# Kernel tuning notes

Hardware: AMD Instinct MI355X
Metric: run time of the kernel (lower is better)

## Reference

```python
import jax, jax.numpy as jnp
import numpy as np

N_A = 50000   # 'user' nodes
N_B = 50000   # 'item' nodes
E = 1000000   # edges per relation
IN, HID, OUT = 128, 128, 64


def setup_inputs() -> dict:
    key = jax.random.key(0)
    ks = jax.random.split(key, 24)
    def glorot(k, shape):
        scale = 1.0 / np.sqrt(shape[0])
        return jax.random.normal(k, shape, jnp.float32) * scale
    inp = {
        "feat_A": jax.random.normal(ks[0], (N_A, IN), jnp.float32),
        "feat_B": jax.random.normal(ks[1], (N_B, IN), jnp.float32),
        "rates_src": jax.random.randint(ks[2], (E,), 0, N_A, jnp.int32),
        "rates_dst": jax.random.randint(ks[3], (E,), 0, N_B, jnp.int32),
        "ratedby_src": jax.random.randint(ks[4], (E,), 0, N_B, jnp.int32),
        "ratedby_dst": jax.random.randint(ks[5], (E,), 0, N_A, jnp.int32),
        "follows_src": jax.random.randint(ks[6], (E,), 0, N_A, jnp.int32),
        "follows_dst": jax.random.randint(ks[7], (E,), 0, N_A, jnp.int32),
        "neg_src": jax.random.randint(ks[8], (E,), 0, N_A, jnp.int32),
        "neg_dst": jax.random.randint(ks[9], (E,), 0, N_B, jnp.int32),
        "W1_rates": glorot(ks[10], (IN, HID)),   "b1_rates": jnp.zeros((HID,), jnp.float32),
        "W1_ratedby": glorot(ks[11], (IN, HID)), "b1_ratedby": jnp.zeros((HID,), jnp.float32),
        "W1_follows": glorot(ks[12], (IN, HID)), "b1_follows": jnp.zeros((HID,), jnp.float32),
        "W2_rates": glorot(ks[13], (HID, OUT)),   "b2_rates": jnp.zeros((OUT,), jnp.float32),
        "W2_ratedby": glorot(ks[14], (HID, OUT)), "b2_ratedby": jnp.zeros((OUT,), jnp.float32),
        "W2_follows": glorot(ks[15], (HID, OUT)), "b2_follows": jnp.zeros((OUT,), jnp.float32),
    }
    return inp


def _graph_conv(x_src, W, b, src, dst, n_src, n_dst):
    # DGL GraphConv, norm='both': D_dst^{-1/2} A D_src^{-1/2} (X W) + b
    ones = jnp.ones(src.shape[0], x_src.dtype)
    deg_out = jnp.maximum(jax.ops.segment_sum(ones, src, num_segments=n_src), 1.0)
    deg_in = jnp.maximum(jax.ops.segment_sum(ones, dst, num_segments=n_dst), 1.0)
    h = (x_src * (deg_out ** -0.5)[:, None]) @ W          # [n_src, d_out]
    agg = jax.ops.segment_sum(h[src], dst, num_segments=n_dst)  # SpMM
    return agg * (deg_in ** -0.5)[:, None] + b


def reference(feat_A, feat_B,
              W1_rates, b1_rates, W1_ratedby, b1_ratedby, W1_follows, b1_follows,
              W2_rates, b2_rates, W2_ratedby, b2_ratedby, W2_follows, b2_follows,
              rates_src, rates_dst, ratedby_src, ratedby_dst,
              follows_src, follows_dst, neg_src, neg_dst):
    # --- RGCN layer 1 (HeteroGraphConv, aggregate='sum') ---
    hB = _graph_conv(feat_A, W1_rates, b1_rates, rates_src, rates_dst, N_A, N_B)
    hA = (_graph_conv(feat_B, W1_ratedby, b1_ratedby, ratedby_src, ratedby_dst, N_B, N_A)
          + _graph_conv(feat_A, W1_follows, b1_follows, follows_src, follows_dst, N_A, N_A))
    hA = jax.nn.relu(hA)
    hB = jax.nn.relu(hB)
    # --- RGCN layer 2 ---
    oB = _graph_conv(hA, W2_rates, b2_rates, rates_src, rates_dst, N_A, N_B)
    oA = (_graph_conv(hB, W2_ratedby, b2_ratedby, ratedby_src, ratedby_dst, N_B, N_A)
          + _graph_conv(hA, W2_follows, b2_follows, follows_src, follows_dst, N_A, N_A))
    # --- HeteroInnerProduct (u_dot_v on etype 'rates') for pos and neg graphs ---
    pos_score = jnp.sum(oA[rates_src] * oB[rates_dst], axis=1, keepdims=True)  # [E, 1]
    neg_score = jnp.sum(oA[neg_src] * oB[neg_dst], axis=1, keepdims=True)      # [E, 1]
    return pos_score, neg_score
```

## Files before the change

kernel.cpp:

```cpp
#include <hip/hip_runtime.h>
#include <hip/hip_fp16.h>
#include <cstddef>
#include <type_traits>

#define N_NODES 50000
#define E_EDGES 1000000
#define NBUCK 196
#define ACHUNK 3907
#define MTILES 3125
#define HB 96
#define HCHUNK 10417
#define GB1 384
#define GB2 256

typedef _Float16 f16x8 __attribute__((ext_vector_type(8)));
typedef float f32x4 __attribute__((ext_vector_type(4)));

__global__ __launch_bounds__(256) void fused0(
        const float* __restrict__ w0, const float* __restrict__ w1,
        const float* __restrict__ w2, const float* __restrict__ w3,
        const float* __restrict__ w4, const float* __restrict__ w5,
        __half* __restrict__ Wt,
        const int* __restrict__ rs, const int* __restrict__ rd,
        const int* __restrict__ bs, const int* __restrict__ bd,
        const int* __restrict__ fs, const int* __restrict__ fd,
        int* __restrict__ bphist) {
    int bx = blockIdx.x;
    if (bx < 6 * HB) {
        __shared__ int l[NBUCK];
        int arr = bx / HB, blk = bx % HB;
        const int* idx = arr == 0 ? rs : arr == 1 ? rd : arr == 2 ? bs
                       : arr == 3 ? bd : arr == 4 ? fs : fd;
        for (int b = threadIdx.x; b < NBUCK; b += 256) l[b] = 0;
        __syncthreads();
        int e0 = blk * HCHUNK;
        int e1 = e0 + HCHUNK; if (e1 > E_EDGES) e1 = E_EDGES;
        for (int i = e0 + threadIdx.x; i < e1; i += 256)
            atomicAdd(&l[((unsigned)idx[i]) >> 8], 1);
        __syncthreads();
        int* dst = bphist + (size_t)(arr * HB + blk) * NBUCK;
        for (int b = threadIdx.x; b < NBUCK; b += 256) dst[b] = l[b];
        return;
    }
    bx -= 6 * HB;
    int m = bx / 16, part = bx % 16;
    const float* W = m == 0 ? w0 : m == 1 ? w1 : m == 2 ? w2 : m == 3 ? w3 : m == 4 ? w4 : w5;
    __half* Tt = Wt + (m < 3 ? m * 16384 : 49152 + (m - 3) * 8192);
    int ncol = m < 3 ? 128 : 64;
    int tot = 128 * ncol;
    for (int i = part * 256 + threadIdx.x; i < tot; i += 16 * 256) {
        int n = i >> 7, k = i & 127;
        Tt[i] = __float2half(W[k * ncol + n]);
    }
}

__global__ void bucket_scan_par(const int* __restrict__ bphist, int* __restrict__ gbase,
                                int* __restrict__ gcur) {
    int arr = blockIdx.x;
    int t = threadIdx.x;
    int c = 0;
    if (t < NBUCK) {
        const int* p = bphist + (size_t)arr * HB * NBUCK + t;
#pragma unroll 8
        for (int blk = 0; blk < HB; blk++) c += p[(size_t)blk * NBUCK];
    }
    int lane = t & 63, wid = t >> 6;
    __shared__ int wsum[4];
    int v = c;
#pragma unroll
    for (int o = 1; o < 64; o <<= 1) { int u = __shfl_up(v, o); if (lane >= o) v += u; }
    if (lane == 63) wsum[wid] = v;
    __syncthreads();
    int base = 0;
    for (int ww = 0; ww < wid; ww++) base += wsum[ww];
    int excl = base + v - c;
    if (t < NBUCK) {
        gbase[arr * (NBUCK + 1) + t] = excl;
        gcur[arr * NBUCK + t] = excl;
    }
    if (t == 255) gbase[arr * (NBUCK + 1) + NBUCK] = base + v;
}

__global__ __launch_bounds__(256) void fused_bin(
        const int* __restrict__ rs, const int* __restrict__ rd,
        const int* __restrict__ bs, const int* __restrict__ bd,
// ... 20 lines not shown
        }
        __syncthreads();
        unsigned* pp = pairs + (size_t)rel * E_EDGES;
        for (int i = e0 + threadIdx.x; i < e1; i += 256) {
            int d = dst[i];
            int b = ((unsigned)d) >> 8;
            int p = lbase[b] + atomicAdd(&lcnt[b], 1);
            pp[p] = ((unsigned)(d & 255) << 16) | (unsigned)src[i];
        }
    } else {
        int rel = y - 3, arr = 2 * rel;
        const int* src = rel == 0 ? rs : rel == 1 ? bs : fs;
        for (int i = e0 + threadIdx.x; i < e1; i += 256)
            atomicAdd(&lcnt[((unsigned)src[i]) >> 8], 1);
        __syncthreads();
        for (int b = threadIdx.x; b < NBUCK; b += 256) {
            lbase[b] = lcnt[b] ? atomicAdd(&gcur[arr * NBUCK + b], lcnt[b]) : 0;
            lcnt[b] = 0;
        }
        __syncthreads();
        unsigned char* sb = sbytes + (size_t)rel * E_EDGES;
        for (int i = e0 + threadIdx.x; i < e1; i += 256) {
            int s = src[i];
            int b = ((unsigned)s) >> 8;
            int p = lbase[b] + atomicAdd(&lcnt[b], 1);
            sb[p] = (unsigned char)(s & 255);
        }
    }
}

__global__ __launch_bounds__(256) void fused_finish(
        const unsigned* __restrict__ pairs, const unsigned char* __restrict__ sbytes,
        const int* __restrict__ gbase, int* __restrict__ row_ptr,
        float* __restrict__ scales, int* __restrict__ col) {
    int y = blockIdx.y, b = blockIdx.x, t = threadIdx.x;
    __shared__ int cnt[256];
    __shared__ int rowbase[256];
    __shared__ int wsum[4];
    if (y < 3) {
        int rel = y, arr = 2 * rel;
        int p0 = gbase[arr * (NBUCK + 1) + b];
        int p1 = gbase[arr * (NBUCK + 1) + b + 1];
        const unsigned char* sb = sbytes + (size_t)rel * E_EDGES;
        cnt[t] = 0;
        __syncthreads();
        for (int i = p0 + t; i < p1; i += 256)
            atomicAdd(&cnt[sb[i]], 1);
        __syncthreads();
        int node = b * 256 + t;
        if (node < N_NODES) {
            int c = cnt[t]; if (c < 1) c = 1;
            scales[(size_t)arr * N_NODES + node] = 1.0f / sqrtf((float)c);
        }
    } else {
        int rel = y - 3, arr = 2 * rel + 1;
        int gb = gbase[arr * (NBUCK + 1) + b];
        int ge = gbase[arr * (NBUCK + 1) + b + 1];
        const unsigned* pp = pairs + (size_t)rel * E_EDGES;
        cnt[t] = 0;
        __syncthreads();
        for (int i = gb + t; i < ge; i += 256)
            atomicAdd(&cnt[pp[i] >> 16], 1);
        __syncthreads();
        int lane = t & 63, wid = t >> 6;
        int c0 = cnt[t];
        int v = c0;
#pragma unroll
        for (int o = 1; o < 64; o <<= 1) { int u = __shfl_up(v, o); if (lane >= o) v += u; }
        if (lane == 63) wsum[wid] = v;
        __syncthreads();
        int base = gb;
        for (int w = 0; w < wid; w++) base += wsum[w];
        int excl = base + v - c0;
        rowbase[t] = excl;
        int node = b * 256 + t;
        if (node <= N_NODES)
            row_ptr[(size_t)rel * (N_NODES + 1) + node] = excl;
        if (node < N_NODES) {
            int c = c0; if (c < 1) c = 1;
            scales[(size_t)arr * N_NODES + node] = 1.0f / sqrtf((float)c);
        }
        cnt[t] = 0;
        __syncthreads();
        int* cl = col + (size_t)rel * E_EDGES;
        for (int i = gb + t; i < ge; i += 256) {
            unsigned p = pp[i];
            int dl = p >> 16;
            int slot = rowbase[dl] + atomicAdd(&cnt[dl], 1);
            cl[slot] = (int)(p & 0xFFFFu);
        }
    }
}

template <int NCOL, typename XT>
__device__ __forceinline__ void gemm_body(const XT* __restrict__ X,
                                          const float* __restrict__ sc,
                                          const __half* __restrict__ Wt,
                                          __half* __restrict__ T,
                                          int bxr, int nblocks) {
    constexpr int NHALF = NCOL / 64;
    int gw = bxr * 4 + ((int)threadIdx.x >> 6);
    int lane = threadIdx.x & 63;
    int half_id = gw % NHALF;
    int mstream = gw / NHALF;
    int nstreams = nblocks * 4 / NHALF;
    int l15 = lane & 15, g = lane >> 4;

    f16x8 b[4][4];
    {
        const __half* wb = Wt + ((size_t)half_id * 64 + l15) * 128 + g * 8;
#pragma unroll
        for (int nt = 0; nt < 4; nt++)
#pragma unroll
            for (int kb = 0; kb < 4; kb++)
                b[nt][kb] = *(const f16x8*)(wb + nt * 16 * 128 + kb * 32);
    }

    for (int mt = mstream; mt < MTILES; mt += nstreams) {
        int m0 = mt * 16;
        f16x8 a[4];
        if constexpr (std::is_same<XT, float>::value) {
            const float* xr = X + (size_t)(m0 + l15) * 128 + g * 8;
#pragma unroll
            for (int kb = 0; kb < 4; kb++) {
                float4 u = *(const float4*)(xr + kb * 32);
                float4 v = *(const float4*)(xr + kb * 32 + 4);
                f16x8 t;
                t[0] = (_Float16)u.x; t[1] = (_Float16)u.y;
                t[2] = (_Float16)u.z; t[3] = (_Float16)u.w;
                t[4] = (_Float16)v.x; t[5] = (_Float16)v.y;
                t[6] = (_Float16)v.z; t[7] = (_Float16)v.w;
                a[kb] = t;
            }
        } else {
            const _Float16* xr = (const _Float16*)X + (size_t)(m0 + l15) * 128 + g * 8;
#pragma unroll
            for (int kb = 0; kb < 4; kb++)
                a[kb] = *(const f16x8*)(xr + kb * 32);
        }
        f32x4 acc[4];
#pragma unroll
        for (int nt = 0; nt < 4; nt++) acc[nt] = (f32x4){0.f, 0.f, 0.f, 0.f};
#pragma unroll
        for (int kb = 0; kb < 4; kb++)
#pragma unroll
            for (int nt = 0; nt < 4; nt++)
                acc[nt] = __builtin_amdgcn_mfma_f32_16x16x32_f16(a[kb], b[nt][kb], acc[nt], 0, 0, 0);
        int mrow = m0 + g * 4;
#pragma unroll
        for (int j = 0; j < 4; j++) {
            float sj = sc[mrow + j];
            __half* tj = T + (size_t)(mrow + j) * NCOL + half_id * 64 + l15;
            tj[0]  = __float2half(acc[0][j] * sj);
            tj[16] = __float2half(acc[1][j] * sj);
            tj[32] = __float2half(acc[2][j] * sj);
            tj[48] = __float2half(acc[3][j] * sj);
        }
    }
}

__global__ __launch_bounds__(256) void gemm_l1(const float* __restrict__ fA,
                                               const float* __restrict__ fB,
                                               const float* __restrict__ scales,
                                               const __half* __restrict__ Wt,
                                               __half* __restrict__ T012) {
    int rel = blockIdx.x / GB1, bxr = blockIdx.x % GB1;
    const float* X = (rel == 1) ? fB : fA;
    const float* sc = scales + (rel == 0 ? 0 : rel == 1 ? 2 * N_NODES : 4 * N_NODES);
    const __half* W = Wt + rel * 16384;
    __half* T = T012 + (size_t)rel * N_NODES * 128;
    gemm_body<128, float>(X, sc, W, T, bxr, GB1);
}

__global__ __launch_bounds__(256) void gemm_l2(const __half* __restrict__ hA,
                                               const __half* __restrict__ hB,
                                               const float* __restrict__ scales,
                                               const __half* __restrict__ Wt,
                                               __half* __restrict__ Tp) {
    int rel = blockIdx.x / GB2, bxr = blockIdx.x % GB2;
    const __half* X = (rel == 1) ? hB : hA;
    const float* sc = scales + (rel == 0 ? 0 : rel == 1 ? 2 * N_NODES : 4 * N_NODES);
    const __half* W = Wt + 49152 + rel * 8192;
    __half* T = Tp + (size_t)rel * N_NODES * 64;
    gemm_body<64, __half>(X, sc, W, T, bxr, GB2);
}

__global__ __launch_bounds__(256) void spmm_l1(
        const int* __restrict__ row_ptr, const int* __restrict__ col,
        const __half* __restrict__ T012, const float* __restrict__ scales,
        const float* __restrict__ b1r, const float* __restrict__ b1rb,
        const float* __restrict__ b1f,
        __half* __restrict__ hB, __half* __restrict__ hA) {
    int w = (blockIdx.x * blockDim.x + threadIdx.x) >> 6;
    int lane = threadIdx.x & 63;
    unsigned loff = (unsigned)lane << 2;
    const char* T0 = (const char*)T012;
    const char* T1 = T0 + (size_t)N_NODES * 256;
    const char* T2 = T1 + (size_t)N_NODES * 256;
#define LDT(B, c) __half22float2(*(const __half2*)((B) + (((unsigned)(c) << 8) + loff)))
    if (w < N_NODES / 2) {
        const int* cl = col;
        int rowA = w * 2, rowB = rowA + 1;
        int eA = row_ptr[rowA], EA = row_ptr[rowA + 1];
        int eB = EA, EB = row_ptr[rowB + 1];
        float axA = 0.f, ayA = 0.f, axB = 0.f, ayB = 0.f;
        while (eA + 4 <= EA && eB + 4 <= EB) {
            int a0 = cl[eA], a1 = cl[eA+1], a2 = cl[eA+2], a3 = cl[eA+3];
            int b0 = cl[eB], b1 = cl[eB+1], b2 = cl[eB+2], b3 = cl[eB+3];
            float2 v0 = LDT(T0, a0), v1 = LDT(T0, a1), v2 = LDT(T0, a2), v3 = LDT(T0, a3);
            float2 u0 = LDT(T0, b0), u1 = LDT(T0, b1), u2 = LDT(T0, b2), u3 = LDT(T0, b3);
            axA += (v0.x + v1.x) + (v2.x + v3.x); ayA += (v0.y + v1.y) + (v2.y + v3.y);
            axB += (u0.x + u1.x) + (u2.x + u3.x); ayB += (u0.y + u1.y) + (u2.y + u3.y);
            eA += 4; eB += 4;
        }
        while (eA + 4 <= EA) {
            int a0 = cl[eA], a1 = cl[eA+1], a2 = cl[eA+2], a3 = cl[eA+3];
            float2 v0 = LDT(T0, a0), v1 = LDT(T0, a1), v2 = LDT(T0, a2), v3 = LDT(T0, a3);
            axA += (v0.x + v1.x) + (v2.x + v3.x); ayA += (v0.y + v1.y) + (v2.y + v3.y);
            eA += 4;
        }
        while (eB + 4 <= EB) {
            int b0 = cl[eB], b1 = cl[eB+1], b2 = cl[eB+2], b3 = cl[eB+3];
            float2 u0 = LDT(T0, b0), u1 = LDT(T0, b1), u2 = LDT(T0, b2), u3 = LDT(T0, b3);
            axB += (u0.x + u1.x) + (u2.x + u3.x); ayB += (u0.y + u1.y) + (u2.y + u3.y);
            eB += 4;
        }
        while (eA < EA && eB < EB) {
            float2 v = LDT(T0, cl[eA]), u = LDT(T0, cl[eB]);
            axA += v.x; ayA += v.y; axB += u.x; ayB += u.y;
            eA++; eB++;
        }
        for (; eA < EA; eA++) { float2 v = LDT(T0, cl[eA]); axA += v.x; ayA += v.y; }
        for (; eB < EB; eB++) { float2 v = LDT(T0, cl[eB]); axB += v.x; ayB += v.y; }
        float bx = b1r[2 * lane], by = b1r[2 * lane + 1];
        float sA = scales[N_NODES + rowA], sB = scales[N_NODES + rowB];
        float ox = fmaxf(fmaf(axA, sA, bx), 0.f), oy = fmaxf(fmaf(ayA, sA, by), 0.f);
        *(__half2*)(hB + (size_t)rowA * 128 + 2 * lane) = __floats2half2_rn(ox, oy);
        ox = fmaxf(fmaf(axB, sB, bx), 0.f); oy = fmaxf(fmaf(ayB, sB, by), 0.f);
        *(__half2*)(hB + (size_t)rowB * 128 + 2 * lane) = __floats2half2_rn(ox, oy);
    } else {
        int r = w - N_NODES / 2;
        const int* rp1 = row_ptr + (N_NODES + 1);
        const int* rp2 = row_ptr + 2 * (N_NODES + 1);
        const int* cl1 = col + E_EDGES;
        const int* cl2 = col + 2 * (size_t)E_EDGES;
        int e1 = rp1[r], E1 = rp1[r + 1];
        int e2 = rp2[r], E2 = rp2[r + 1];
        float a1x = 0.f, a1y = 0.f, a2x = 0.f, a2y = 0.f;
        while (e1 + 4 <= E1 && e2 + 4 <= E2) {
            int a0 = cl1[e1], a1 = cl1[e1+1], a2 = cl1[e1+2], a3 = cl1[e1+3];
            int b0 = cl2[e2], b1 = cl2[e2+1], b2 = cl2[e2+2], b3 = cl2[e2+3];
            float2 v0 = LDT(T1, a0), v1 = LDT(T1, a1), v2 = LDT(T1, a2), v3 = LDT(T1, a3);
            float2 u0 = LDT(T2, b0), u1 = LDT(T2, b1), u2 = LDT(T2, b2), u3 = LDT(T2, b3);
            a1x += (v0.x + v1.x) + (v2.x + v3.x); a1y += (v0.y + v1.y) + (v2.y + v3.y);
            a2x += (u0.x + u1.x) + (u2.x + u3.x); a2y += (u0.y + u1.y) + (u2.y + u3.y);
            e1 += 4; e2 += 4;
        }
        while (e1 + 4 <= E1) {
            int a0 = cl1[e1], a1 = cl1[e1+1], a2 = cl1[e1+2], a3 = cl1[e1+3];
            float2 v0 = LDT(T1, a0), v1 = LDT(T1, a1), v2 = LDT(T1, a2), v3 = LDT(T1, a3);
            a1x += (v0.x + v1.x) + (v2.x + v3.x); a1y += (v0.y + v1.y) + (v2.y + v3.y);
            e1 += 4;
        }
        while (e2 + 4 <= E2) {
            int b0 = cl2[e2], b1 = cl2[e2+1], b2 = cl2[e2+2], b3 = cl2[e2+3];
            float2 u0 = LDT(T2, b0), u1 = LDT(T2, b1), u2 = LDT(T2, b2), u3 = LDT(T2, b3);
            a2x += (u0.x + u1.x) + (u2.x + u3.x); a2y += (u0.y + u1.y) + (u2.y + u3.y);
            e2 += 4;
        }
        while (e1 < E1 && e2 < E2) {
            float2 v = LDT(T1, cl1[e1]), u = LDT(T2, cl2[e2]);
            a1x += v.x; a1y += v.y; a2x += u.x; a2y += u.y;
            e1++; e2++;
        }
        for (; e1 < E1; e1++) { float2 v = LDT(T1, cl1[e1]); a1x += v.x; a1y += v.y; }
        for (; e2 < E2; e2++) { float2 v = LDT(T2, cl2[e2]); a2x += v.x; a2y += v.y; }
        float s1 = scales[3 * N_NODES + r], s2 = scales[5 * N_NODES + r];
        float ox = a1x * s1 + a2x * s2 + b1rb[2 * lane] + b1f[2 * lane];
        float oy = a1y * s1 + a2y * s2 + b1rb[2 * lane + 1] + b1f[2 * lane + 1];
        ox = fmaxf(ox, 0.f); oy = fmaxf(oy, 0.f);
        *(__half2*)(hA + (size_t)r * 128 + 2 * lane) = __floats2half2_rn(ox, oy);
    }
#undef LDT
}

__global__ __launch_bounds__(256) void spmm_l2(
        const int* __restrict__ row_ptr, const int* __restrict__ col,
        const __half* __restrict__ Tp, const float* __restrict__ scales,
        const float* __restrict__ b2r, const float* __restrict__ b2rb,
        const float* __restrict__ b2f,
        __half* __restrict__ oB, __half* __restrict__ oA) {
    int g = (blockIdx.x * blockDim.x + threadIdx.x) >> 5;
    int l2 = threadIdx.x & 31;
    unsigned loff = (unsigned)l2 << 2;
    const char* T0 = (const char*)Tp;
    const char* T1 = T0 + (size_t)N_NODES * 128;
    const char* T2 = T1 + (size_t)N_NODES * 128;
#define LDT(B, c) __half22float2(*(const __half2*)((B) + (((unsigned)(c) << 7) + loff)))
    if (g < N_NODES / 2) {
        const int* cl = col;
        int rowA = g * 2, rowB = rowA + 1;
        int eA = row_ptr[rowA], EA = row_ptr[rowA + 1];
        int eB = EA, EB = row_ptr[rowB + 1];
        float axA = 0.f, ayA = 0.f, axB = 0.f, ayB = 0.f;
        while (eA + 4 <= EA && eB + 4 <= EB) {
            int a0 = cl[eA], a1 = cl[eA+1], a2 = cl[eA+2], a3 = cl[eA+3];
            int b0 = cl[eB], b1 = cl[eB+1], b2 = cl[eB+2], b3 = cl[eB+3];
            float2 v0 = LDT(T0, a0), v1 = LDT(T0, a1), v2 = LDT(T0, a2), v3 = LDT(T0, a3);
            float2 u0 = LDT(T0, b0), u1 = LDT(T0, b1), u2 = LDT(T0, b2), u3 = LDT(T0, b3);
            axA += (v0.x + v1.x) + (v2.x + v3.x); ayA += (v0.y + v1.y) + (v2.y + v3.y);
            axB += (u0.x + u1.x) + (u2.x + u3.x); ayB += (u0.y + u1.y) + (u2.y + u3.y);
            eA += 4; eB += 4;
        }
        while (eA + 4 <= EA) {
            int a0 = cl[eA], a1 = cl[eA+1], a2 = cl[eA+2], a3 = cl[eA+3];
            float2 v0 = LDT(T0, a0), v1 = LDT(T0, a1), v2 = LDT(T0, a2), v3 = LDT(T0, a3);
            axA += (v0.x + v1.x) + (v2.x + v3.x); ayA += (v0.y + v1.y) + (v2.y + v3.y);
            eA += 4;
        }
        while (eB + 4 <= EB) {
            int b0 = cl[eB], b1 = cl[eB+1], b2 = cl[eB+2], b3 = cl[eB+3];
            float2 u0 = LDT(T0, b0), u1 = LDT(T0, b1), u2 = LDT(T0, b2), u3 = LDT(T0, b3);
            axB += (u0.x + u1.x) + (u2.x + u3.x); ayB += (u0.y + u1.y) + (u2.y + u3.y);
            eB += 4;
        }
        while (eA < EA && eB < EB) {
            float2 v = LDT(T0, cl[eA]), u = LDT(T0, cl[eB]);
            axA += v.x; ayA += v.y; axB += u.x; ayB += u.y;
            eA++; eB++;
        }
        for (; eA < EA; eA++) { float2 v = LDT(T0, cl[eA]); axA += v.x; ayA += v.y; }
        for (; eB < EB; eB++) { float2 v = LDT(T0, cl[eB]); axB += v.x; ayB += v.y; }
        float bx = b2r[2 * l2], by = b2r[2 * l2 + 1];
        float sA = scales[N_NODES + rowA], sB = scales[N_NODES + rowB];
        *(__half2*)(oB + (size_t)rowA * 64 + 2 * l2) =
            __floats2half2_rn(fmaf(axA, sA, bx), fmaf(ayA, sA, by));
        *(__half2*)(oB + (size_t)rowB * 64 + 2 * l2) =
            __floats2half2_rn(fmaf(axB, sB, bx), fmaf(ayB, sB, by));
    } else {
        int r = g - N_NODES / 2;
        const int* rp1 = row_ptr + (N_NODES + 1);
        const int* rp2 = row_ptr + 2 * (N_NODES + 1);
        const int* cl1 = col + E_EDGES;
        const int* cl2 = col + 2 * (size_t)E_EDGES;
        int e1 = rp1[r], E1 = rp1[r + 1];
        int e2 = rp2[r], E2 = rp2[r + 1];
        float a1x = 0.f, a1y = 0.f, a2x = 0.f, a2y = 0.f;
        while (e1 + 4 <= E1 && e2 + 4 <= E2) {
            int a0 = cl1[e1], a1 = cl1[e1+1], a2 = cl1[e1+2], a3 = cl1[e1+3];
            int b0 = cl2[e2], b1 = cl2[e2+1], b2 = cl2[e2+2], b3 = cl2[e2+3];
            float2 v0 = LDT(T1, a0), v1 = LDT(T1, a1), v2 = LDT(T1, a2), v3 = LDT(T1, a3);
            float2 u0 = LDT(T2, b0), u1 = LDT(T2, b1), u2 = LDT(T2, b2), u3 = LDT(T2, b3);
            a1x += (v0.x + v1.x) + (v2.x + v3.x); a1y += (v0.y + v1.y) + (v2.y + v3.y);
            a2x += (u0.x + u1.x) + (u2.x + u3.x); a2y += (u0.y + u1.y) + (u2.y + u3.y);
            e1 += 4; e2 += 4;
        }
        while (e1 + 4 <= E1) {
            int a0 = cl1[e1], a1 = cl1[e1+1], a2 = cl1[e1+2], a3 = cl1[e1+3];
            float2 v0 = LDT(T1, a0), v1 = LDT(T1, a1), v2 = LDT(T1, a2), v3 = LDT(T1, a3);
            a1x += (v0.x + v1.x) + (v2.x + v3.x); a1y += (v0.y + v1.y) + (v2.y + v3.y);
            e1 += 4;
        }
        while (e2 + 4 <= E2) {
            int b0 = cl2[e2], b1 = cl2[e2+1], b2 = cl2[e2+2], b3 = cl2[e2+3];
            float2 u0 = LDT(T2, b0), u1 = LDT(T2, b1), u2 = LDT(T2, b2), u3 = LDT(T2, b3);
            a2x += (u0.x + u1.x) + (u2.x + u3.x); a2y += (u0.y + u1.y) + (u2.y + u3.y);
            e2 += 4;
        }
        while (e1 < E1 && e2 < E2) {
            float2 v = LDT(T1, cl1[e1]), u = LDT(T2, cl2[e2]);
            a1x += v.x; a1y += v.y; a2x += u.x; a2y += u.y;
            e1++; e2++;
        }
        for (; e1 < E1; e1++) { float2 v = LDT(T1, cl1[e1]); a1x += v.x; a1y += v.y; }
        for (; e2 < E2; e2++) { float2 v = LDT(T2, cl2[e2]); a2x += v.x; a2y += v.y; }
        float s1 = scales[3 * N_NODES + r], s2 = scales[5 * N_NODES + r];
        float ox = a1x * s1 + a2x * s2 + b2rb[2 * l2] + b2f[2 * l2];
        float oy = a1y * s1 + a2y * s2 + b2rb[2 * l2 + 1] + b2f[2 * l2 + 1];
        *(__half2*)(oA + (size_t)r * 64 + 2 * l2) = __floats2half2_rn(ox, oy);
    }
#undef LDT
}

__global__ __launch_bounds__(256) void score2(const __half* __restrict__ oA,
                                              const __half* __restrict__ oB,
                                              const int* __restrict__ ps,
                                              const int* __restrict__ pd,
                                              const int* __restrict__ ns,
                                              const int* __restrict__ nd,
                                              float* __restrict__ out) {
    int g = (blockIdx.x * blockDim.x + threadIdx.x) >> 4;
    int l = threadIdx.x & 15;
    int ng = (gridDim.x * blockDim.x) >> 4;
    const char* A = (const char*)oA;
    const char* B = (const char*)oB;
    unsigned loff = (unsigned)l << 3;
#define SCORE_LOOP(SRC, DST, OUT)                                               \
    for (int e0 = g * 2; e0 < E_EDGES; e0 += ng * 2) {                          \
        int e1 = e0 + 1;                                                        \
        int s0 = SRC[e0], d0 = DST[e0], s1 = SRC[e1], d1 = DST[e1];             \
        union { uint2 u; __half2 h[2]; } a0, b0, a1, b1;                        \
        a0.u = *(const uint2*)(A + (((unsigned)s0 << 7) + loff));               \
        b0.u = *(const uint2*)(B + (((unsigned)d0 << 7) + loff));               \
        a1.u = *(const uint2*)(A + (((unsigned)s1 << 7) + loff));               \
        b1.u = *(const uint2*)(B + (((unsigned)d1 << 7) + loff));               \
// ... 28 lines not shown
    const int* ratedby_src  = (const int*)d_in[4];
    const int* ratedby_dst  = (const int*)d_in[5];
    const int* follows_src  = (const int*)d_in[6];
    const int* follows_dst  = (const int*)d_in[7];
    const int* neg_src      = (const int*)d_in[8];
    const int* neg_dst      = (const int*)d_in[9];
    const float* W1_rates   = (const float*)d_in[10];
    const float* b1_rates   = (const float*)d_in[11];
    const float* W1_ratedby = (const float*)d_in[12];
    const float* b1_ratedby = (const float*)d_in[13];
    const float* W1_follows = (const float*)d_in[14];
    const float* b1_follows = (const float*)d_in[15];
    const float* W2_rates   = (const float*)d_in[16];
    const float* b2_rates   = (const float*)d_in[17];
    const float* W2_ratedby = (const float*)d_in[18];
    const float* b2_ratedby = (const float*)d_in[19];
    const float* W2_follows = (const float*)d_in[20];
    const float* b2_follows = (const float*)d_in[21];

    const int N = N_NODES, E = E_EDGES;

    char* ws = (char*)d_ws;
    size_t off = 0;
    auto alloc = [&](size_t bytes) -> void* {
        void* p = ws + off;
        off += (bytes + 255) & ~(size_t)255;
        return p;
    };
    float* scales = (float*)alloc((size_t)6 * N * 4);
    int* row_ptr  = (int*)alloc((size_t)3 * (N + 1) * 4);
    int* bphist   = (int*)alloc((size_t)6 * HB * NBUCK * 4);
    int* gbase    = (int*)alloc((size_t)6 * (NBUCK + 1) * 4);
    int* gcur     = (int*)alloc((size_t)6 * NBUCK * 4);
    int* col      = (int*)alloc((size_t)3 * E * 4);
    unsigned* pairs = (unsigned*)alloc((size_t)3 * E * 4);
    unsigned char* sbytes = (unsigned char*)alloc((size_t)3 * E);
    __half* T012  = (__half*)alloc((size_t)3 * N * 128 * 2);
    __half* Tp    = (__half*)alloc((size_t)3 * N * 64 * 2);
    __half* hA    = (__half*)alloc((size_t)N * 128 * 2);
    __half* hB    = (__half*)alloc((size_t)N * 128 * 2);
    __half* oA    = (__half*)alloc((size_t)N * 64 * 2);
    __half* oB    = (__half*)alloc((size_t)N * 64 * 2);
    __half* Wt    = (__half*)alloc((size_t)(3 * 128 * 128 + 3 * 128 * 64) * 2);
    (void)ws_size;

    fused0<<<6 * HB + 96, 256, 0, stream>>>(W1_rates, W1_ratedby, W1_follows,
                                            W2_rates, W2_ratedby, W2_follows, Wt,
                                            rates_src, rates_dst, ratedby_src,
                                            ratedby_dst, follows_src, follows_dst,
                                            bphist);
    bucket_scan_par<<<6, 256, 0, stream>>>(bphist, gbase, gcur);
    fused_bin<<<dim3(256, 6), 256, 0, stream>>>(rates_src, rates_dst, ratedby_src,
                                                ratedby_dst, follows_src, follows_dst,
                                                gcur, pairs, sbytes);
    fused_finish<<<dim3(NBUCK, 6), 256, 0, stream>>>(pairs, sbytes, gbase,
                                                     row_ptr, scales, col);

    gemm_l1<<<3 * GB1, 256, 0, stream>>>(feat_A, feat_B, scales, Wt, T012);
    spmm_l1<<<(3 * N / 2) / 4, 256, 0, stream>>>(row_ptr, col, T012, scales,
                                                 b1_rates, b1_ratedby, b1_follows,
                                                 hB, hA);
    gemm_l2<<<3 * GB2, 256, 0, stream>>>(hA, hB, scales, Wt, Tp);
    spmm_l2<<<(3 * N / 2) / 8, 256, 0, stream>>>(row_ptr, col, Tp, scales,
                                                 b2_rates, b2_ratedby, b2_follows,
                                                 oB, oA);
    score2<<<8192, 256, 0, stream>>>(oA, oB, rates_src, rates_dst,
                                     neg_src, neg_dst, (float*)d_out);
}
```

Measured before the change: 358.9 us.

## Aggregate-then-transform layer 1, concatenate ratedby/follows GEMM, use 16-bit column indices

Layer 1 now aggregates half-precision input features with per-source degree scaling first, then runs the dense GEMM with bias and ReLU fused into its epilogue. The two A-side relations are merged into a single K=256 GEMM over concatenated aggregates and stacked weights. Feature conversion to fp16 is folded into the first kernel, CSR column indices shrink to 16-bit, and workspace buffers are aliased to reduce memory traffic. In exchange the scalar-scale loads in the SpMM become per-edge gathers, and two GEMM launches replace one.

```diff
diff --git a/kernel.cpp b/kernel.cpp
--- a/kernel.cpp
+++ b/kernel.cpp
@@ -1,7 +1,6 @@
 #include <hip/hip_runtime.h>
 #include <hip/hip_fp16.h>
 #include <cstddef>
-#include <type_traits>
 
 #define N_NODES 50000
 #define E_EDGES 1000000
@@ -10,17 +9,18 @@
 #define MTILES 3125
 #define HB 96
 #define HCHUNK 10417
-#define GB1 384
-#define GB2 256
 
 typedef _Float16 f16x8 __attribute__((ext_vector_type(8)));
 typedef float f32x4 __attribute__((ext_vector_type(4)));
 
+
 __global__ __launch_bounds__(256) void fused0(
-        const float* __restrict__ w0, const float* __restrict__ w1,
-        const float* __restrict__ w2, const float* __restrict__ w3,
-        const float* __restrict__ w4, const float* __restrict__ w5,
+        const float* __restrict__ w1r, const float* __restrict__ w1rb,
+        const float* __restrict__ w1f, const float* __restrict__ w2r,
+        const float* __restrict__ w2rb, const float* __restrict__ w2f,
         __half* __restrict__ Wt,
+        const float* __restrict__ fA, const float* __restrict__ fB,
+        __half* __restrict__ XAh, __half* __restrict__ XBh,
         const int* __restrict__ rs, const int* __restrict__ rd,
         const int* __restrict__ bs, const int* __restrict__ bd,
         const int* __restrict__ fs, const int* __restrict__ fd,
@@ -43,14 +43,39 @@
         return;
     }
     bx -= 6 * HB;
-    int m = bx / 16, part = bx % 16;
-    const float* W = m == 0 ? w0 : m == 1 ? w1 : m == 2 ? w2 : m == 3 ? w3 : m == 4 ? w4 : w5;
-    __half* Tt = Wt + (m < 3 ? m * 16384 : 49152 + (m - 3) * 8192);
-    int ncol = m < 3 ? 128 : 64;
-    int tot = 128 * ncol;
-    for (int i = part * 256 + threadIdx.x; i < tot; i += 16 * 256) {
-        int n = i >> 7, k = i & 127;
-        Tt[i] = __float2half(W[k * ncol + n]);
+    if (bx < 96) {
+        int m = bx / 16, part = bx % 16;
+        if (m == 0) {
+            for (int i = part * 256 + threadIdx.x; i < 16384; i += 4096) {
+                int n = i >> 7, k = i & 127;
+                Wt[i] = __float2half(w1r[k * 128 + n]);
+            }
+        } else if (m == 1 || m == 2) {
+            const float* W = (m == 1) ? w1rb : w1f;
+            int koff = (m == 2) ? 128 : 0;
+            for (int i = part * 256 + threadIdx.x; i < 16384; i += 4096) {
+                int n = i >> 7, k = i & 127;
+                Wt[16384 + n * 256 + koff + k] = __float2half(W[k * 128 + n]);
+            }
+        } else {
+            const float* W = m == 3 ? w2r : m == 4 ? w2rb : w2f;
+            __half* dst = Wt + 49152 + (m - 3) * 8192;
+            for (int i = part * 256 + threadIdx.x; i < 8192; i += 4096) {
+                int n = i >> 7, k = i & 127;
+                dst[i] = __float2half(W[k * 64 + n]);
+            }
+        }
+        return;
+    }
+    bx -= 96;
+    for (int q = bx * 256 + threadIdx.x; q < 3200000; q += 256 * 256) {
+        bool isA = q < 1600000;
+        int qq = isA ? q : q - 1600000;
+        float4 v = ((const float4*)(isA ? fA : fB))[qq];
+        union { __half2 h[2]; uint2 u; } cv;
+        cv.h[0] = __floats2half2_rn(v.x, v.y);
+        cv.h[1] = __floats2half2_rn(v.z, v.w);
+        ((uint2*)(isA ? XAh : XBh))[qq] = cv.u;
     }
 }
 
@@ -137,7 +162,7 @@
 __global__ __launch_bounds__(256) void fused_finish(
         const unsigned* __restrict__ pairs, const unsigned char* __restrict__ sbytes,
         const int* __restrict__ gbase, int* __restrict__ row_ptr,
-        float* __restrict__ scales, int* __restrict__ col) {
+        float* __restrict__ scales, unsigned short* __restrict__ col) {
     int y = blockIdx.y, b = blockIdx.x, t = threadIdx.x;
     __shared__ int cnt[256];
     __shared__ int rowbase[256];
@@ -187,23 +212,107 @@
         }
         cnt[t] = 0;
         __syncthreads();
-        int* cl = col + (size_t)rel * E_EDGES;
+        unsigned short* cl = col + (size_t)rel * E_EDGES;
         for (int i = gb + t; i < ge; i += 256) {
             unsigned p = pp[i];
             int dl = p >> 16;
             int slot = rowbase[dl] + atomicAdd(&cnt[dl], 1);
-            cl[slot] = (int)(p & 0xFFFFu);
-        }
-    }
-}
-
-template <int NCOL, typename XT>
-__device__ __forceinline__ void gemm_body(const XT* __restrict__ X,
+            cl[slot] = (unsigned short)(p & 0xFFFFu);
+        }
+    }
+}
+
+__global__ __launch_bounds__(256) void spmm_l1(
+        const int* __restrict__ row_ptr, const unsigned short* __restrict__ col,
+        const __half* __restrict__ XAh, const __half* __restrict__ XBh,
+        const float* __restrict__ scales,
+        __half* __restrict__ agg0, __half* __restrict__ aggA) {
+    int t = (blockIdx.x * blockDim.x + threadIdx.x) >> 6;
+    int lane = threadIdx.x & 63;
+    unsigned loff = (unsigned)lane << 2;
+    const char* XA = (const char*)XAh;
+    const char* XB = (const char*)XBh;
+#define LDX(B, c) __half22float2(*(const __half2*)((B) + (((unsigned)(c) << 8) + loff)))
+    if (t < 25000) {
+        const unsigned short* cl = col;
+        const float* se = scales;
+        int rowA = t * 2, rowB = rowA + 1;
+        int eA = row_ptr[rowA], EA = row_ptr[rowA + 1];
+        int eB = EA, EB = row_ptr[rowB + 1];
+        float axA = 0.f, ayA = 0.f, axB = 0.f, ayB = 0.f;
+        while (eA + 4 <= EA && eB + 4 <= EB) {
+            int a0 = cl[eA], a1 = cl[eA+1], a2 = cl[eA+2], a3 = cl[eA+3];
+            int b0 = cl[eB], b1 = cl[eB+1], b2 = cl[eB+2], b3 = cl[eB+3];
+            float sa0 = se[a0], sa1 = se[a1], sa2 = se[a2], sa3 = se[a3];
+            float sb0 = se[b0], sb1 = se[b1], sb2 = se[b2], sb3 = se[b3];
+            float2 v0 = LDX(XA, a0), v1 = LDX(XA, a1), v2 = LDX(XA, a2), v3 = LDX(XA, a3);
+            float2 u0 = LDX(XA, b0), u1 = LDX(XA, b1), u2 = LDX(XA, b2), u3 = LDX(XA, b3);
+            axA = fmaf(sa0, v0.x, fmaf(sa1, v1.x, fmaf(sa2, v2.x, fmaf(sa3, v3.x, axA))));
+            ayA = fmaf(sa0, v0.y, fmaf(sa1, v1.y, fmaf(sa2, v2.y, fmaf(sa3, v3.y, ayA))));
+            axB = fmaf(sb0, u0.x, fmaf(sb1, u1.x, fmaf(sb2, u2.x, fmaf(sb3, u3.x, axB))));
+            ayB = fmaf(sb0, u0.y, fmaf(sb1, u1.y, fmaf(sb2, u2.y, fmaf(sb3, u3.y, ayB))));
+            eA += 4; eB += 4;
+        }
+        for (; eA < EA; eA++) {
+            int c = cl[eA]; float s = se[c]; float2 v = LDX(XA, c);
+            axA = fmaf(s, v.x, axA); ayA = fmaf(s, v.y, ayA);
+        }
+        for (; eB < EB; eB++) {
+            int c = cl[eB]; float s = se[c]; float2 v = LDX(XA, c);
+            axB = fmaf(s, v.x, axB); ayB = fmaf(s, v.y, ayB);
+        }
+        float sA = scales[N_NODES + rowA], sB = scales[N_NODES + rowB];
+        *(__half2*)(agg0 + (size_t)rowA * 128 + 2 * lane) = __floats2half2_rn(axA * sA, ayA * sA);
+        *(__half2*)(agg0 + (size_t)rowB * 128 + 2 * lane) = __floats2half2_rn(axB * sB, ayB * sB);
+    } else {
+        int r = t - 25000;
+        const int* rp1 = row_ptr + (N_NODES + 1);
+        const int* rp2 = row_ptr + 2 * (N_NODES + 1);
+        const unsigned short* cl1 = col + E_EDGES;
+        const unsigned short* cl2 = col + 2 * (size_t)E_EDGES;
+        const float* se1 = scales + 2 * N_NODES;
+        const float* se2 = scales + 4 * N_NODES;
+        int e1 = rp1[r], E1 = rp1[r + 1];
+        int e2 = rp2[r], E2 = rp2[r + 1];
+        float a1x = 0.f, a1y = 0.f, a2x = 0.f, a2y = 0.f;
+        while (e1 + 4 <= E1 && e2 + 4 <= E2) {
+            int a0 = cl1[e1], a1 = cl1[e1+1], a2 = cl1[e1+2], a3 = cl1[e1+3];
+            int b0 = cl2[e2], b1 = cl2[e2+1], b2 = cl2[e2+2], b3 = cl2[e2+3];
+            float sa0 = se1[a0], sa1 = se1[a1], sa2 = se1[a2], sa3 = se1[a3];
+            float sb0 = se2[b0], sb1 = se2[b1], sb2 = se2[b2], sb3 = se2[b3];
+            float2 v0 = LDX(XB, a0), v1 = LDX(XB, a1), v2 = LDX(XB, a2), v3 = LDX(XB, a3);
+            float2 u0 = LDX(XA, b0), u1 = LDX(XA, b1), u2 = LDX(XA, b2), u3 = LDX(XA, b3);
+            a1x = fmaf(sa0, v0.x, fmaf(sa1, v1.x, fmaf(sa2, v2.x, fmaf(sa3, v3.x, a1x))));
+            a1y = fmaf(sa0, v0.y, fmaf(sa1, v1.y, fmaf(sa2, v2.y, fmaf(sa3, v3.y, a1y))));
+            a2x = fmaf(sb0, u0.x, fmaf(sb1, u1.x, fmaf(sb2, u2.x, fmaf(sb3, u3.x, a2x))));
+            a2y = fmaf(sb0, u0.y, fmaf(sb1, u1.y, fmaf(sb2, u2.y, fmaf(sb3, u3.y, a2y))));
+            e1 += 4; e2 += 4;
+        }
+        for (; e1 < E1; e1++) {
+            int c = cl1[e1]; float s = se1[c]; float2 v = LDX(XB, c);
+            a1x = fmaf(s, v.x, a1x); a1y = fmaf(s, v.y, a1y);
+        }
+        for (; e2 < E2; e2++) {
+            int c = cl2[e2]; float s = se2[c]; float2 v = LDX(XA, c);
+            a2x = fmaf(s, v.x, a2x); a2y = fmaf(s, v.y, a2y);
+        }
+        float s3 = scales[3 * N_NODES + r], s5 = scales[5 * N_NODES + r];
+        *(__half2*)(aggA + (size_t)r * 256 + 2 * lane) = __floats2half2_rn(a1x * s3, a1y * s3);
+        *(__half2*)(aggA + (size_t)r * 256 + 128 + 2 * lane) = __floats2half2_rn(a2x * s5, a2y * s5);
+    }
+#undef LDX
+}
+
+template <int NCOL, int KD, int EPI>
+__device__ __forceinline__ void gemm_core(const __half* __restrict__ X,
+                                          const __half* __restrict__ Wt,
+                                          __half* __restrict__ OUT,
                                           const float* __restrict__ sc,
-                                          const __half* __restrict__ Wt,
-                                          __half* __restrict__ T,
+                                          const float* __restrict__ bs1,
+                                          const float* __restrict__ bs2,
                                           int bxr, int nblocks) {
     constexpr int NHALF = NCOL / 64;
+    constexpr int KB = KD / 32;
     int gw = bxr * 4 + ((int)threadIdx.x >> 6);
     int lane = threadIdx.x & 63;
     int half_id = gw % NHALF;
@@ -211,70 +320,68 @@
     int nstreams = nblocks * 4 / NHALF;
     int l15 = lane & 15, g = lane >> 4;
 
-    f16x8 b[4][4];
-    {
-        const __half* wb = Wt + ((size_t)half_id * 64 + l15) * 128 + g * 8;
-#pragma unroll
-        for (int nt = 0; nt < 4; nt++)
-#pragma unroll
-            for (int kb = 0; kb < 4; kb++)
-                b[nt][kb] = *(const f16x8*)(wb + nt * 16 * 128 + kb * 32);
+    f16x8 b[4][KB];
+    float bias_nt[4];
+#pragma unroll
+    for (int nt = 0; nt < 4; nt++) {
+        int colv = half_id * 64 + nt * 16 + l15;
+        const __half* wb = Wt + (size_t)colv * KD + g * 8;
+#pragma unroll
+        for (int kb = 0; kb < KB; kb++)
+            b[nt][kb] = *(const f16x8*)(wb + kb * 32);
+        if (EPI == 1) bias_nt[nt] = bs1[colv];
+        if (EPI == 2) bias_nt[nt] = bs1[colv] + bs2[colv];
     }
 
     for (int mt = mstream; mt < MTILES; mt += nstreams) {
         int m0 = mt * 16;
-        f16x8 a[4];
-        if constexpr (std::is_same<XT, float>::value) {
-            const float* xr = X + (size_t)(m0 + l15) * 128 + g * 8;
-#pragma unroll
-            for (int kb = 0; kb < 4; kb++) {
-                float4 u = *(const float4*)(xr + kb * 32);
-                float4 v = *(const float4*)(xr + kb * 32 + 4);
-                f16x8 t;
-                t[0] = (_Float16)u.x; t[1] = (_Float16)u.y;
-                t[2] = (_Float16)u.z; t[3] = (_Float16)u.w;
-                t[4] = (_Float16)v.x; t[5] = (_Float16)v.y;
-                t[6] = (_Float16)v.z; t[7] = (_Float16)v.w;
-                a[kb] = t;
-            }
-        } else {
-            const _Float16* xr = (const _Float16*)X + (size_t)(m0 + l15) * 128 + g * 8;
-#pragma unroll
-            for (int kb = 0; kb < 4; kb++)
-                a[kb] = *(const f16x8*)(xr + kb * 32);
-        }
+        const _Float16* xr = (const _Float16*)X + (size_t)(m0 + l15) * KD + g * 8;
+        f16x8 a[KB];
+#pragma unroll
+        for (int kb = 0; kb < KB; kb++)
+            a[kb] = *(const f16x8*)(xr + kb * 32);
         f32x4 acc[4];
 #pragma unroll
         for (int nt = 0; nt < 4; nt++) acc[nt] = (f32x4){0.f, 0.f, 0.f, 0.f};
 #pragma unroll
-        for (int kb = 0; kb < 4; kb++)
+        for (int kb = 0; kb < KB; kb++)
 #pragma unroll
             for (int nt = 0; nt < 4; nt++)
                 acc[nt] = __builtin_amdgcn_mfma_f32_16x16x32_f16(a[kb], b[nt][kb], acc[nt], 0, 0, 0);
         int mrow = m0 + g * 4;
 #pragma unroll
         for (int j = 0; j < 4; j++) {
-            float sj = sc[mrow + j];
-            __half* tj = T + (size_t)(mrow + j) * NCOL + half_id * 64 + l15;
-            tj[0]  = __float2half(acc[0][j] * sj);
-            tj[16] = __float2half(acc[1][j] * sj);
-            tj[32] = __float2half(acc[2][j] * sj);
-            tj[48] = __float2half(acc[3][j] * sj);
-        }
-    }
-}
-
-__global__ __launch_bounds__(256) void gemm_l1(const float* __restrict__ fA,
-                                               const float* __restrict__ fB,
-                                               const float* __restrict__ scales,
+            int row = mrow + j;
+            float sj = (EPI == 0) ? sc[row] : 0.f;
+            __half* tj = OUT + (size_t)row * NCOL + half_id * 64 + l15;
+#pragma unroll
+            for (int nt = 0; nt < 4; nt++) {
+                float v = acc[nt][j];
+                if (EPI == 0) v *= sj;
+                else { v += bias_nt[nt]; v = fmaxf(v, 0.f); }
+                tj[nt * 16] = __float2half(v);
+            }
+        }
+    }
+}
+
+#define GBH 256
+#define GBA 384
+#define GB2 256
+
+__global__ __launch_bounds__(256) void gemm_hB(const __half* __restrict__ agg0,
                                                const __half* __restrict__ Wt,
-                                               __half* __restrict__ T012) {
-    int rel = blockIdx.x / GB1, bxr = blockIdx.x % GB1;
-    const float* X = (rel == 1) ? fB : fA;
-    const float* sc = scales + (rel == 0 ? 0 : rel == 1 ? 2 * N_NODES : 4 * N_NODES);
-    const __half* W = Wt + rel * 16384;
-    __half* T = T012 + (size_t)rel * N_NODES * 128;
-    gemm_body<128, float>(X, sc, W, T, bxr, GB1);
+                                               const float* __restrict__ b1r,
+                                               __half* __restrict__ hB) {
+    gemm_core<128, 128, 1>(agg0, Wt, hB, nullptr, b1r, nullptr, blockIdx.x, GBH);
+}
+
+__global__ __launch_bounds__(256) void gemm_hA(const __half* __restrict__ aggA,
+                                               const __half* __restrict__ Wt,
+                                               const float* __restrict__ b1rb,
+                                               const float* __restrict__ b1f,
+                                               __half* __restrict__ hA) {
+    gemm_core<128, 256, 2>(aggA, Wt + 16384, hA, nullptr, b1rb, b1f, blockIdx.x, GBA);
 }
 
 __global__ __launch_bounds__(256) void gemm_l2(const __half* __restrict__ hA,
@@ -285,112 +392,12 @@
     int rel = blockIdx.x / GB2, bxr = blockIdx.x % GB2;
     const __half* X = (rel == 1) ? hB : hA;
     const float* sc = scales + (rel == 0 ? 0 : rel == 1 ? 2 * N_NODES : 4 * N_NODES);
-    const __half* W = Wt + 49152 + rel * 8192;
-    __half* T = Tp + (size_t)rel * N_NODES * 64;
-    gemm_body<64, __half>(X, sc, W, T, bxr, GB2);
-}
-
-__global__ __launch_bounds__(256) void spmm_l1(
-        const int* __restrict__ row_ptr, const int* __restrict__ col,
-        const __half* __restrict__ T012, const float* __restrict__ scales,
-        const float* __restrict__ b1r, const float* __restrict__ b1rb,
-        const float* __restrict__ b1f,
-        __half* __restrict__ hB, __half* __restrict__ hA) {
-    int w = (blockIdx.x * blockDim.x + threadIdx.x) >> 6;
-    int lane = threadIdx.x & 63;
-    unsigned loff = (unsigned)lane << 2;
-    const char* T0 = (const char*)T012;
-    const char* T1 = T0 + (size_t)N_NODES * 256;
-    const char* T2 = T1 + (size_t)N_NODES * 256;
-#define LDT(B, c) __half22float2(*(const __half2*)((B) + (((unsigned)(c) << 8) + loff)))
-    if (w < N_NODES / 2) {
-        const int* cl = col;
-        int rowA = w * 2, rowB = rowA + 1;
-        int eA = row_ptr[rowA], EA = row_ptr[rowA + 1];
-        int eB = EA, EB = row_ptr[rowB + 1];
-        float axA = 0.f, ayA = 0.f, axB = 0.f, ayB = 0.f;
-        while (eA + 4 <= EA && eB + 4 <= EB) {
-            int a0 = cl[eA], a1 = cl[eA+1], a2 = cl[eA+2], a3 = cl[eA+3];
-            int b0 = cl[eB], b1 = cl[eB+1], b2 = cl[eB+2], b3 = cl[eB+3];
-            float2 v0 = LDT(T0, a0), v1 = LDT(T0, a1), v2 = LDT(T0, a2), v3 = LDT(T0, a3);
-            float2 u0 = LDT(T0, b0), u1 = LDT(T0, b1), u2 = LDT(T0, b2), u3 = LDT(T0, b3);
-            axA += (v0.x + v1.x) + (v2.x + v3.x); ayA += (v0.y + v1.y) + (v2.y + v3.y);
-            axB += (u0.x + u1.x) + (u2.x + u3.x); ayB += (u0.y + u1.y) + (u2.y + u3.y);
-            eA += 4; eB += 4;
-        }
-        while (eA + 4 <= EA) {
-            int a0 = cl[eA], a1 = cl[eA+1], a2 = cl[eA+2], a3 = cl[eA+3];
-            float2 v0 = LDT(T0, a0), v1 = LDT(T0, a1), v2 = LDT(T0, a2), v3 = LDT(T0, a3);
-            axA += (v0.x + v1.x) + (v2.x + v3.x); ayA += (v0.y + v1.y) + (v2.y + v3.y);
-            eA += 4;
-        }
-        while (eB + 4 <= EB) {
-            int b0 = cl[eB], b1 = cl[eB+1], b2 = cl[eB+2], b3 = cl[eB+3];
-            float2 u0 = LDT(T0, b0), u1 = LDT(T0, b1), u2 = LDT(T0, b2), u3 = LDT(T0, b3);
-            axB += (u0.x + u1.x) + (u2.x + u3.x); ayB += (u0.y + u1.y) + (u2.y + u3.y);
-            eB += 4;
-        }
-        while (eA < EA && eB < EB) {
-            float2 v = LDT(T0, cl[eA]), u = LDT(T0, cl[eB]);
-            axA += v.x; ayA += v.y; axB += u.x; ayB += u.y;
-            eA++; eB++;
-        }
-        for (; eA < EA; eA++) { float2 v = LDT(T0, cl[eA]); axA += v.x; ayA += v.y; }
-        for (; eB < EB; eB++) { float2 v = LDT(T0, cl[eB]); axB += v.x; ayB += v.y; }
-        float bx = b1r[2 * lane], by = b1r[2 * lane + 1];
-        float sA = scales[N_NODES + rowA], sB = scales[N_NODES + rowB];
-        float ox = fmaxf(fmaf(axA, sA, bx), 0.f), oy = fmaxf(fmaf(ayA, sA, by), 0.f);
-        *(__half2*)(hB + (size_t)rowA * 128 + 2 * lane) = __floats2half2_rn(ox, oy);
-        ox = fmaxf(fmaf(axB, sB, bx), 0.f); oy = fmaxf(fmaf(ayB, sB, by), 0.f);
-        *(__half2*)(hB + (size_t)rowB * 128 + 2 * lane) = __floats2half2_rn(ox, oy);
-    } else {
-        int r = w - N_NODES / 2;
-        const int* rp1 = row_ptr + (N_NODES + 1);
-        const int* rp2 = row_ptr + 2 * (N_NODES + 1);
-        const int* cl1 = col + E_EDGES;
-        const int* cl2 = col + 2 * (size_t)E_EDGES;
-        int e1 = rp1[r], E1 = rp1[r + 1];
-        int e2 = rp2[r], E2 = rp2[r + 1];
-        float a1x = 0.f, a1y = 0.f, a2x = 0.f, a2y = 0.f;
-        while (e1 + 4 <= E1 && e2 + 4 <= E2) {
-            int a0 = cl1[e1], a1 = cl1[e1+1], a2 = cl1[e1+2], a3 = cl1[e1+3];
-            int b0 = cl2[e2], b1 = cl2[e2+1], b2 = cl2[e2+2], b3 = cl2[e2+3];
-            float2 v0 = LDT(T1, a0), v1 = LDT(T1, a1), v2 = LDT(T1, a2), v3 = LDT(T1, a3);
-            float2 u0 = LDT(T2, b0), u1 = LDT(T2, b1), u2 = LDT(T2, b2), u3 = LDT(T2, b3);
-            a1x += (v0.x + v1.x) + (v2.x + v3.x); a1y += (v0.y + v1.y) + (v2.y + v3.y);
-            a2x += (u0.x + u1.x) + (u2.x + u3.x); a2y += (u0.y + u1.y) + (u2.y + u3.y);
-            e1 += 4; e2 += 4;
-        }
-        while (e1 + 4 <= E1) {
-            int a0 = cl1[e1], a1 = cl1[e1+1], a2 = cl1[e1+2], a3 = cl1[e1+3];
-            float2 v0 = LDT(T1, a0), v1 = LDT(T1, a1), v2 = LDT(T1, a2), v3 = LDT(T1, a3);
-            a1x += (v0.x + v1.x) + (v2.x + v3.x); a1y += (v0.y + v1.y) + (v2.y + v3.y);
-            e1 += 4;
-        }
-        while (e2 + 4 <= E2) {
-            int b0 = cl2[e2], b1 = cl2[e2+1], b2 = cl2[e2+2], b3 = cl2[e2+3];
-            float2 u0 = LDT(T2, b0), u1 = LDT(T2, b1), u2 = LDT(T2, b2), u3 = LDT(T2, b3);
-            a2x += (u0.x + u1.x) + (u2.x + u3.x); a2y += (u0.y + u1.y) + (u2.y + u3.y);
-            e2 += 4;
-        }
-        while (e1 < E1 && e2 < E2) {
-            float2 v = LDT(T1, cl1[e1]), u = LDT(T2, cl2[e2]);
-            a1x += v.x; a1y += v.y; a2x += u.x; a2y += u.y;
-            e1++; e2++;
-        }
-        for (; e1 < E1; e1++) { float2 v = LDT(T1, cl1[e1]); a1x += v.x; a1y += v.y; }
-        for (; e2 < E2; e2++) { float2 v = LDT(T2, cl2[e2]); a2x += v.x; a2y += v.y; }
-        float s1 = scales[3 * N_NODES + r], s2 = scales[5 * N_NODES + r];
-        float ox = a1x * s1 + a2x * s2 + b1rb[2 * lane] + b1f[2 * lane];
-        float oy = a1y * s1 + a2y * s2 + b1rb[2 * lane + 1] + b1f[2 * lane + 1];
-        ox = fmaxf(ox, 0.f); oy = fmaxf(oy, 0.f);
-        *(__half2*)(hA + (size_t)r * 128 + 2 * lane) = __floats2half2_rn(ox, oy);
-    }
-#undef LDT
+    gemm_core<64, 128, 0>(X, Wt + 49152 + rel * 8192, Tp + (size_t)rel * N_NODES * 64,
+                          sc, nullptr, nullptr, bxr, GB2);
 }
 
 __global__ __launch_bounds__(256) void spmm_l2(
-        const int* __restrict__ row_ptr, const int* __restrict__ col,
+        const int* __restrict__ row_ptr, const unsigned short* __restrict__ col,
         const __half* __restrict__ Tp, const float* __restrict__ scales,
         const float* __restrict__ b2r, const float* __restrict__ b2rb,
         const float* __restrict__ b2f,
@@ -403,7 +410,7 @@
     const char* T2 = T1 + (size_t)N_NODES * 128;
 #define LDT(B, c) __half22float2(*(const __half2*)((B) + (((unsigned)(c) << 7) + loff)))
     if (g < N_NODES / 2) {
-        const int* cl = col;
+        const unsigned short* cl = col;
         int rowA = g * 2, rowB = rowA + 1;
         int eA = row_ptr[rowA], EA = row_ptr[rowA + 1];
         int eB = EA, EB = row_ptr[rowB + 1];
@@ -417,23 +424,6 @@
             axB += (u0.x + u1.x) + (u2.x + u3.x); ayB += (u0.y + u1.y) + (u2.y + u3.y);
             eA += 4; eB += 4;
         }
-        while (eA + 4 <= EA) {
-            int a0 = cl[eA], a1 = cl[eA+1], a2 = cl[eA+2], a3 = cl[eA+3];
-            float2 v0 = LDT(T0, a0), v1 = LDT(T0, a1), v2 = LDT(T0, a2), v3 = LDT(T0, a3);
-            axA += (v0.x + v1.x) + (v2.x + v3.x); ayA += (v0.y + v1.y) + (v2.y + v3.y);
-            eA += 4;
-        }
-        while (eB + 4 <= EB) {
-            int b0 = cl[eB], b1 = cl[eB+1], b2 = cl[eB+2], b3 = cl[eB+3];
-            float2 u0 = LDT(T0, b0), u1 = LDT(T0, b1), u2 = LDT(T0, b2), u3 = LDT(T0, b3);
-            axB += (u0.x + u1.x) + (u2.x + u3.x); ayB += (u0.y + u1.y) + (u2.y + u3.y);
-            eB += 4;
-        }
-        while (eA < EA && eB < EB) {
-            float2 v = LDT(T0, cl[eA]), u = LDT(T0, cl[eB]);
-            axA += v.x; ayA += v.y; axB += u.x; ayB += u.y;
-            eA++; eB++;
-        }
         for (; eA < EA; eA++) { float2 v = LDT(T0, cl[eA]); axA += v.x; ayA += v.y; }
         for (; eB < EB; eB++) { float2 v = LDT(T0, cl[eB]); axB += v.x; ayB += v.y; }
         float bx = b2r[2 * l2], by = b2r[2 * l2 + 1];
@@ -446,8 +436,8 @@
         int r = g - N_NODES / 2;
         const int* rp1 = row_ptr + (N_NODES + 1);
         const int* rp2 = row_ptr + 2 * (N_NODES + 1);
-        const int* cl1 = col + E_EDGES;
-        const int* cl2 = col + 2 * (size_t)E_EDGES;
+        const unsigned short* cl1 = col + E_EDGES;
+        const unsigned short* cl2 = col + 2 * (size_t)E_EDGES;
         int e1 = rp1[r], E1 = rp1[r + 1];
         int e2 = rp2[r], E2 = rp2[r + 1];
         float a1x = 0.f, a1y = 0.f, a2x = 0.f, a2y = 0.f;
@@ -459,23 +449,6 @@
             a1x += (v0.x + v1.x) + (v2.x + v3.x); a1y += (v0.y + v1.y) + (v2.y + v3.y);
             a2x += (u0.x + u1.x) + (u2.x + u3.x); a2y += (u0.y + u1.y) + (u2.y + u3.y);
             e1 += 4; e2 += 4;
-        }
-        while (e1 + 4 <= E1) {
-            int a0 = cl1[e1], a1 = cl1[e1+1], a2 = cl1[e1+2], a3 = cl1[e1+3];
-            float2 v0 = LDT(T1, a0), v1 = LDT(T1, a1), v2 = LDT(T1, a2), v3 = LDT(T1, a3);
-            a1x += (v0.x + v1.x) + (v2.x + v3.x); a1y += (v0.y + v1.y) + (v2.y + v3.y);
-            e1 += 4;
-        }
-        while (e2 + 4 <= E2) {
-            int b0 = cl2[e2], b1 = cl2[e2+1], b2 = cl2[e2+2], b3 = cl2[e2+3];
-            float2 u0 = LDT(T2, b0), u1 = LDT(T2, b1), u2 = LDT(T2, b2), u3 = LDT(T2, b3);
-            a2x += (u0.x + u1.x) + (u2.x + u3.x); a2y += (u0.y + u1.y) + (u2.y + u3.y);
-            e2 += 4;
-        }
-        while (e1 < E1 && e2 < E2) {
-            float2 v = LDT(T1, cl1[e1]), u = LDT(T2, cl2[e2]);
-            a1x += v.x; a1y += v.y; a2x += u.x; a2y += u.y;
-            e1++; e2++;
         }
         for (; e1 < E1; e1++) { float2 v = LDT(T1, cl1[e1]); a1x += v.x; a1y += v.y; }
         for (; e2 < E2; e2++) { float2 v = LDT(T2, cl2[e2]); a2x += v.x; a2y += v.y; }
@@ -570,23 +543,29 @@
     int* bphist   = (int*)alloc((size_t)6 * HB * NBUCK * 4);
     int* gbase    = (int*)alloc((size_t)6 * (NBUCK + 1) * 4);
     int* gcur     = (int*)alloc((size_t)6 * NBUCK * 4);
-    int* col      = (int*)alloc((size_t)3 * E * 4);
-    unsigned* pairs = (unsigned*)alloc((size_t)3 * E * 4);
-    unsigned char* sbytes = (unsigned char*)alloc((size_t)3 * E);
-    __half* T012  = (__half*)alloc((size_t)3 * N * 128 * 2);
-    __half* Tp    = (__half*)alloc((size_t)3 * N * 64 * 2);
-    __half* hA    = (__half*)alloc((size_t)N * 128 * 2);
-    __half* hB    = (__half*)alloc((size_t)N * 128 * 2);
-    __half* oA    = (__half*)alloc((size_t)N * 64 * 2);
-    __half* oB    = (__half*)alloc((size_t)N * 64 * 2);
-    __half* Wt    = (__half*)alloc((size_t)(3 * 128 * 128 + 3 * 128 * 64) * 2);
+    unsigned short* col = (unsigned short*)alloc((size_t)3 * E * 2);
+    char* region1 = (char*)alloc((size_t)16 * 1024 * 1024);
+    unsigned* pairs = (unsigned*)region1;
+    unsigned char* sbytes = (unsigned char*)(pairs + (size_t)3 * E);
+    __half* agg0 = (__half*)region1;
+    char* regionX = (char*)alloc((size_t)N * 128 * 2);
+    __half* XAh = (__half*)regionX;
+    __half* oA  = (__half*)regionX;
+    __half* oB  = oA + (size_t)N * 64;
+    char* regionA = (char*)alloc((size_t)N * 256 * 2);
+    __half* aggA = (__half*)regionA;
+    __half* Tp   = (__half*)regionA;
+    __half* XBh  = (__half*)alloc((size_t)N * 128 * 2);
+    __half* hA   = (__half*)alloc((size_t)N * 128 * 2);
+    __half* hB   = (__half*)alloc((size_t)N * 128 * 2);
+    __half* Wt   = (__half*)alloc((size_t)73728 * 2);
     (void)ws_size;
 
-    fused0<<<6 * HB + 96, 256, 0, stream>>>(W1_rates, W1_ratedby, W1_follows,
-                                            W2_rates, W2_ratedby, W2_follows, Wt,
-                                            rates_src, rates_dst, ratedby_src,
-                                            ratedby_dst, follows_src, follows_dst,
-                                            bphist);
+    fused0<<<6 * HB + 96 + 256, 256, 0, stream>>>(
+        W1_rates, W1_ratedby, W1_follows, W2_rates, W2_ratedby, W2_follows, Wt,
+        feat_A, feat_B, XAh, XBh,
+        rates_src, rates_dst, ratedby_src, ratedby_dst, follows_src, follows_dst,
+        bphist);
     bucket_scan_par<<<6, 256, 0, stream>>>(bphist, gbase, gcur);
     fused_bin<<<dim3(256, 6), 256, 0, stream>>>(rates_src, rates_dst, ratedby_src,
                                                 ratedby_dst, follows_src, follows_dst,
@@ -594,10 +573,10 @@
     fused_finish<<<dim3(NBUCK, 6), 256, 0, stream>>>(pairs, sbytes, gbase,
                                                      row_ptr, scales, col);
 
-    gemm_l1<<<3 * GB1, 256, 0, stream>>>(feat_A, feat_B, scales, Wt, T012);
-    spmm_l1<<<(3 * N / 2) / 4, 256, 0, stream>>>(row_ptr, col, T012, scales,
-                                                 b1_rates, b1_ratedby, b1_follows,
-                                                 hB, hA);
+    spmm_l1<<<(3 * N / 2) / 4, 256, 0, stream>>>(row_ptr, col, XAh, XBh, scales,
+                                                 agg0, aggA);
+    gemm_hB<<<GBH, 256, 0, stream>>>(agg0, Wt, b1_rates, hB);
+    gemm_hA<<<GBA, 256, 0, stream>>>(aggA, Wt, b1_ratedby, b1_follows, hA);
     gemm_l2<<<3 * GB2, 256, 0, stream>>>(hA, hB, scales, Wt, Tp);
     spmm_l2<<<(3 * N / 2) / 8, 256, 0, stream>>>(row_ptr, col, Tp, scales,
                                                  b2_rates, b2_ratedby, b2_follows,
```

Result: slower. 402.2 us (+12.1%).
